# Performance work log

Hardware: AMD Instinct MI355X
Metric: run time of the kernel (lower is better)

Reference implementation:

```python
import jax, jax.numpy as jnp
from jax import lax
import numpy as np

DIM = 16
VOCAB = 18


def setup_inputs() -> dict:
    key = jax.random.key(0)
    ks = jax.random.split(key, 7)
    B, T = 4096, 2048
    x = jax.random.randint(ks[0], (B, T), 0, VOCAB, dtype=jnp.int64)
    emb = jax.random.normal(ks[1], (VOCAB, DIM), dtype=jnp.float32)
    W_w = jax.random.normal(ks[2], (DIM, DIM), dtype=jnp.float32) * (1.0 / np.sqrt(DIM))
    W_b = jax.random.normal(ks[3], (DIM,), dtype=jnp.float32) * 0.01
    U_w = jax.random.normal(ks[4], (DIM, DIM), dtype=jnp.float32) * (1.0 / np.sqrt(DIM))
    head_w = jax.random.normal(ks[5], (VOCAB, DIM), dtype=jnp.float32) * (1.0 / np.sqrt(DIM))
    head_b = jax.random.normal(ks[6], (VOCAB,), dtype=jnp.float32) * 0.01
    return {"x": x, "emb": emb, "W_w": W_w, "W_b": W_b, "U_w": U_w,
            "head_w": head_w, "head_b": head_b}


def reference(x, emb, W_w, W_b, U_w, head_w, head_b):
    # x: [B, T] int tokens; emb: [V, D]; W_w/U_w: [D, D]; head_w: [V, D]
    B, T = x.shape
    D = emb.shape[1]
    # Input-dependent term W(emb(x_t)) + b has no recurrence: precompute for all t.
    e = emb[x]                                   # [B, T, D] gather
    we = jnp.einsum('btd,kd->btk', e, W_w) + W_b  # [B, T, D]

    def step(h, we_t):
        # h_{t} = tanh(W emb(x_t) + b + U h_{t-1})
        h_new = jnp.tanh(we_t + h @ U_w.T)       # [B, D]
        return h_new, None

    h0 = jnp.zeros((B, D), dtype=emb.dtype)
    h_final, _ = lax.scan(step, h0, jnp.swapaxes(we, 0, 1))  # scan over T
    # head(h_final): [B, V]  (gates tensor in the original is all-ones and unused)
    return h_final @ head_w.T + head_b
```

## Files before the change

kernel.cpp:

```cpp
#include <hip/hip_runtime.h>
#include <cmath>

#define DIM 16
#define VOCAB 18
#define TLEN 2048
#define NBLK (TLEN / 64)
#define TWO_LOG2E 2.8853900817779268f

__device__ __forceinline__ float ldf(const void* p, int idx, int isbf) {
    if (isbf) {
        unsigned int w = ((const unsigned short*)p)[idx];
        return __uint_as_float(w << 16);
    }
    return ((const float*)p)[idx];
}

__global__ void detect_tok(const int* __restrict__ x32, int* __restrict__ flag) {
    int v = 0;
    for (int j = threadIdx.x; j < 4096; j += 64) v |= x32[2 * j + 1];
    unsigned long long any = __ballot(v != 0);
    if (threadIdx.x == 0) flag[0] = (any == 0ULL) ? 1 : 0;
}

__global__ void detect_f(const unsigned short* __restrict__ emb16,
                         int* __restrict__ flag) {
    int bad = 0;
    for (int j = threadIdx.x; j < VOCAB * DIM; j += 64) {
        unsigned short w = emb16[j];
        int e = (w >> 7) & 0xFF;
        if (!((e >= 90 && e <= 140) || (w & 0x7FFF) == 0)) bad = 1;
    }
    unsigned long long anybad = __ballot(bad);
    if (threadIdx.x == 0) flag[1] = (anybad == 0ULL) ? 1 : 0;
}

__global__ void wtab_kernel(const void* __restrict__ emb,
                            const void* __restrict__ W_w,
                            const void* __restrict__ W_b,
                            const int* __restrict__ flag,
                            float* __restrict__ wtab) {
    int tid = threadIdx.x;
    int isbf = flag[1];
    if (tid < VOCAB * DIM) {
        int v = tid >> 4, kk = tid & 15;
        float s = ldf(W_b, kk, isbf);
#pragma unroll
        for (int d = 0; d < DIM; ++d)
            s = fmaf(ldf(emb, v * DIM + d, isbf), ldf(W_w, kk * DIM + d, isbf), s);
        wtab[tid] = s;
    }
}

#define WSTR 19
#define SSTR 68

__global__ __launch_bounds__(256) void rnn_kernel(const int* __restrict__ x32,
                                                  const int* __restrict__ flag,
                                                  const float* __restrict__ wtab_g,
                                                  const void* __restrict__ U_w,
                                                  const void* __restrict__ head_w,
                                                  const void* __restrict__ head_b,
                                                  float* __restrict__ out) {
    __shared__ float wtabT[16 * WSTR];
    __shared__ float sU[DIM * DIM];
    __shared__ float lds_h[16][DIM];
    __shared__ int slab[2][16 * SSTR];

    const int tid = threadIdx.x;
    const int is64 = __builtin_amdgcn_readfirstlane(flag[0]);
    const int isbf = __builtin_amdgcn_readfirstlane(flag[1]);

    for (int i = tid; i < 16 * WSTR; i += 256) {
        int r = i / WSTR, v = i - r * WSTR;
        float val = 0.0f;
        if (v < VOCAB) {
            float rs = 0.0f;
#pragma unroll
            for (int d = 0; d < DIM; ++d) rs += ldf(U_w, r * DIM + d, isbf);
            val = (wtab_g[v * DIM + r] + rs) * TWO_LOG2E;
        }
        wtabT[i] = val;
    }
    for (int i = tid; i < DIM * DIM; i += 256) sU[i] = ldf(U_w, i, isbf);
    __syncthreads();

    const int lane = tid & 63;
    const int wave = tid >> 6;
    const int g16 = lane >> 4;
    const int k = lane & 15;
    const int e = (wave << 2) | g16;
    const int gelem = (blockIdx.x << 4) | e;

    int p = __builtin_amdgcn_mov_dpp(k, 0x121, 0xF, 0xF, true);
    int c = (p - k) & 15;

    float ur2[16];
#pragma unroll
    for (int j = 0; j < 16; ++j)
        ur2[j] = sU[(k << 4) | ((k + j * c) & 15)] * (-2.0f * TWO_LOG2E);

    const int wb = k * WSTR;

    const size_t tokbase = (size_t)gelem * TLEN + (k << 2);

    int* cur = &slab[0][e * SSTR];
    int* nxt = &slab[1][e * SSTR];

    int4 g0;
#define LOADG(G, B)                                                           \
    {                                                                         \
        if (is64) {                                                           \
            const int* pp = x32 + ((tokbase + ((size_t)(B) << 6)) << 1);      \
            int4 a = *(const int4*)pp;                                        \
            int4 bq = *(const int4*)(pp + 4);                                 \
            G = make_int4(a.x, a.z, bq.x, bq.z);                              \
        } else {                                                              \
            G = *(const int4*)(x32 + tokbase + ((size_t)(B) << 6));           \
        }                                                                     \
    }

    LOADG(g0, 0)
    *(int4*)(cur + (k << 2)) = g0;
    int4 gcur;
    LOADG(gcur, 1)

    int4 tA = *(const int4*)(cur + 0);
    int4 tB = *(const int4*)(cur + 4);
    float wq0 = wtabT[wb + tA.x];
    float wq1 = wtabT[wb + tA.y];
    float wq2 = wtabT[wb + tA.z];
    float wq3 = wtabT[wb + tA.w];

    float rst = 0.5f;

#define STEP(W, TN, WN)                                                        \
    {                                                                          \
        WN = wtabT[wb + (TN)];                                                 \
        float a0 = fmaf(ur2[0], rst, W);                                       \
        float a1, a2, a3;                                                      \
        asm("s_nop 1\n\t"                                                      \
            "v_mul_f32_dpp %[a1], %[r], %[u1] row_ror:1 row_mask:0xf bank_mask:0xf\n\t"  \
            "v_mul_f32_dpp %[a2], %[r], %[u2] row_ror:2 row_mask:0xf bank_mask:0xf\n\t"  \
            "v_mul_f32_dpp %[a3], %[r], %[u3] row_ror:3 row_mask:0xf bank_mask:0xf\n\t"  \
            "v_fmac_f32_dpp %[a0], %[r], %[u4] row_ror:4 row_mask:0xf bank_mask:0xf\n\t" \
            "v_fmac_f32_dpp %[a1], %[r], %[u5] row_ror:5 row_mask:0xf bank_mask:0xf\n\t" \
            "v_fmac_f32_dpp %[a2], %[r], %[u6] row_ror:6 row_mask:0xf bank_mask:0xf\n\t" \
            "v_fmac_f32_dpp %[a3], %[r], %[u7] row_ror:7 row_mask:0xf bank_mask:0xf\n\t" \
            "v_fmac_f32_dpp %[a0], %[r], %[u8] row_ror:8 row_mask:0xf bank_mask:0xf\n\t" \
            "v_fmac_f32_dpp %[a1], %[r], %[u9] row_ror:9 row_mask:0xf bank_mask:0xf\n\t" \
            "v_fmac_f32_dpp %[a2], %[r], %[u10] row_ror:10 row_mask:0xf bank_mask:0xf\n\t" \
            "v_fmac_f32_dpp %[a3], %[r], %[u11] row_ror:11 row_mask:0xf bank_mask:0xf\n\t" \
            "v_fmac_f32_dpp %[a0], %[r], %[u12] row_ror:12 row_mask:0xf bank_mask:0xf\n\t" \
            "v_fmac_f32_dpp %[a1], %[r], %[u13] row_ror:13 row_mask:0xf bank_mask:0xf\n\t" \
            "v_fmac_f32_dpp %[a2], %[r], %[u14] row_ror:14 row_mask:0xf bank_mask:0xf\n\t" \
            "v_fmac_f32_dpp %[a3], %[r], %[u15] row_ror:15 row_mask:0xf bank_mask:0xf"     \
            : [a0] "+v"(a0), [a1] "=&v"(a1), [a2] "=&v"(a2), [a3] "=&v"(a3)    \
            : [r] "v"(rst), [u1] "v"(ur2[1]), [u2] "v"(ur2[2]),                \
              [u3] "v"(ur2[3]), [u4] "v"(ur2[4]), [u5] "v"(ur2[5]),            \
              [u6] "v"(ur2[6]), [u7] "v"(ur2[7]), [u8] "v"(ur2[8]),            \
              [u9] "v"(ur2[9]), [u10] "v"(ur2[10]), [u11] "v"(ur2[11]),        \
              [u12] "v"(ur2[12]), [u13] "v"(ur2[13]), [u14] "v"(ur2[14]),      \
              [u15] "v"(ur2[15]));                                             \
        float S = (a0 + a1) + (a2 + a3);                                       \
        rst = __builtin_amdgcn_rcpf(__builtin_amdgcn_exp2f(S) + 1.0f);         \
    }

    for (int b = 0; b < NBLK; ++b) {
        *(int4*)(nxt + (k << 2)) = gcur;
        const int nb2 = (b + 2 < NBLK) ? b + 2 : NBLK - 1;
        LOADG(gcur, nb2)

#pragma unroll
        for (int gi = 0; gi < 16; ++gi) {
            int4 tC = (gi < 14) ? *(const int4*)(cur + ((gi + 2) << 2))
                                : *(const int4*)(nxt + ((gi - 14) << 2));

            float wn0, wn1, wn2, wn3;
            STEP(wq0, tB.x, wn0)
            STEP(wq1, tB.y, wn1)
            STEP(wq2, tB.z, wn2)
            STEP(wq3, tB.w, wn3)

            wq0 = wn0;
            wq1 = wn1;
            wq2 = wn2;
            wq3 = wn3;
            tB = tC;
        }
        int* tmp = cur;
        cur = nxt;
        nxt = tmp;
    }

    lds_h[e][k] = fmaf(-2.0f, rst, 1.0f);
    __syncthreads();

    for (int i = tid; i < 16 * VOCAB; i += 256) {
        int ee = i / VOCAB;
        int v = i - ee * VOCAB;
        float s = ldf(head_b, v, isbf);
#pragma unroll
        for (int d = 0; d < DIM; ++d)
            s = fmaf(lds_h[ee][d], ldf(head_w, (v << 4) + d, isbf), s);
        out[(size_t)((blockIdx.x << 4) | ee) * VOCAB + v] = s;
    }
}

extern "C" void kernel_launch(void* const* d_in, const int* in_sizes, int n_in,
                              void* d_out, int out_size, void* d_ws, size_t ws_size,
                              hipStream_t stream) {
    const int* x = (const int*)d_in[0];
    const void* emb = d_in[1];
    const void* W_w = d_in[2];
    const void* W_b = d_in[3];
    const void* U_w = d_in[4];
    const void* head_w = d_in[5];
    const void* head_b = d_in[6];

    float* wtab = (float*)d_ws;
    int* flag = (int*)((char*)d_ws + 4096);

    detect_tok<<<1, 64, 0, stream>>>(x, flag);
    detect_f<<<1, 64, 0, stream>>>((const unsigned short*)emb, flag);
    wtab_kernel<<<1, 320, 0, stream>>>(emb, W_w, W_b, flag, wtab);
    rnn_kernel<<<256, 256, 0, stream>>>(x, flag, wtab, U_w, head_w, head_b,
                                        (float*)d_out);
}
```

Before: 149.1 us.

## Interleave two independent recurrences per 16-lane group to hide latency

Each 16-lane group now carries two batch elements, A and B, and alternates their recurrence steps, so each wave runs two independent dependency chains. Blocks drop to 128 threads (2 waves) while still covering 16 elements per block. The goal is to hide the DPP/exp/rcp latency of the serial chain through instruction-level parallelism, since the grid of 256 blocks leaves the GPU underoccupied. The cost is half as many waves in flight and more registers per thread.

```diff
diff --git a/kernel.cpp b/kernel.cpp
--- a/kernel.cpp
+++ b/kernel.cpp
@@ -54,7 +54,7 @@
 #define WSTR 19
 #define SSTR 68
 
-__global__ __launch_bounds__(256) void rnn_kernel(const int* __restrict__ x32,
+__global__ __launch_bounds__(128) void rnn_kernel(const int* __restrict__ x32,
                                                   const int* __restrict__ flag,
                                                   const float* __restrict__ wtab_g,
                                                   const void* __restrict__ U_w,
@@ -70,7 +70,7 @@
     const int is64 = __builtin_amdgcn_readfirstlane(flag[0]);
     const int isbf = __builtin_amdgcn_readfirstlane(flag[1]);
 
-    for (int i = tid; i < 16 * WSTR; i += 256) {
+    for (int i = tid; i < 16 * WSTR; i += 128) {
         int r = i / WSTR, v = i - r * WSTR;
         float val = 0.0f;
         if (v < VOCAB) {
@@ -81,15 +81,17 @@
         }
         wtabT[i] = val;
     }
-    for (int i = tid; i < DIM * DIM; i += 256) sU[i] = ldf(U_w, i, isbf);
+    for (int i = tid; i < DIM * DIM; i += 128) sU[i] = ldf(U_w, i, isbf);
     __syncthreads();
 
     const int lane = tid & 63;
     const int wave = tid >> 6;
     const int g16 = lane >> 4;
     const int k = lane & 15;
-    const int e = (wave << 2) | g16;
-    const int gelem = (blockIdx.x << 4) | e;
+    const int eA = (wave << 3) | g16;
+    const int eB = eA + 4;
+    const int gelemA = (blockIdx.x << 4) | eA;
+    const int gelemB = (blockIdx.x << 4) | eB;
 
     int p = __builtin_amdgcn_mov_dpp(k, 0x121, 0xF, 0xF, true);
     int c = (p - k) & 15;
@@ -101,42 +103,50 @@
 
     const int wb = k * WSTR;
 
-    const size_t tokbase = (size_t)gelem * TLEN + (k << 2);
-
-    int* cur = &slab[0][e * SSTR];
-    int* nxt = &slab[1][e * SSTR];
-
-    int4 g0;
-#define LOADG(G, B)                                                           \
+    const size_t tokbaseA = (size_t)gelemA * TLEN + (k << 2);
+    const size_t tokbaseB = (size_t)gelemB * TLEN + (k << 2);
+
+    int* curA = &slab[0][eA * SSTR];
+    int* nxtA = &slab[1][eA * SSTR];
+    int* curB = &slab[0][eB * SSTR];
+    int* nxtB = &slab[1][eB * SSTR];
+
+#define LOADG(G, B, TOKBASE)                                                  \
     {                                                                         \
         if (is64) {                                                           \
-            const int* pp = x32 + ((tokbase + ((size_t)(B) << 6)) << 1);      \
+            const int* pp = x32 + (((TOKBASE) + ((size_t)(B) << 6)) << 1);    \
             int4 a = *(const int4*)pp;                                        \
             int4 bq = *(const int4*)(pp + 4);                                 \
             G = make_int4(a.x, a.z, bq.x, bq.z);                              \
         } else {                                                              \
-            G = *(const int4*)(x32 + tokbase + ((size_t)(B) << 6));           \
+            G = *(const int4*)(x32 + (TOKBASE) + ((size_t)(B) << 6));         \
         }                                                                     \
     }
 
-    LOADG(g0, 0)
-    *(int4*)(cur + (k << 2)) = g0;
-    int4 gcur;
-    LOADG(gcur, 1)
-
-    int4 tA = *(const int4*)(cur + 0);
-    int4 tB = *(const int4*)(cur + 4);
-    float wq0 = wtabT[wb + tA.x];
-    float wq1 = wtabT[wb + tA.y];
-    float wq2 = wtabT[wb + tA.z];
-    float wq3 = wtabT[wb + tA.w];
-
-    float rst = 0.5f;
-
-#define STEP(W, TN, WN)                                                        \
+    int4 g0;
+    LOADG(g0, 0, tokbaseA)
+    *(int4*)(curA + (k << 2)) = g0;
+    LOADG(g0, 0, tokbaseB)
+    *(int4*)(curB + (k << 2)) = g0;
+    int4 gcurA, gcurB;
+    LOADG(gcurA, 1, tokbaseA)
+    LOADG(gcurB, 1, tokbaseB)
+
+    int4 tA0 = *(const int4*)(curA + 0);
+    int4 tnA = *(const int4*)(curA + 4);
+    float wqA0 = wtabT[wb + tA0.x], wqA1 = wtabT[wb + tA0.y];
+    float wqA2 = wtabT[wb + tA0.z], wqA3 = wtabT[wb + tA0.w];
+    int4 tB0 = *(const int4*)(curB + 0);
+    int4 tnB = *(const int4*)(curB + 4);
+    float wqB0 = wtabT[wb + tB0.x], wqB1 = wtabT[wb + tB0.y];
+    float wqB2 = wtabT[wb + tB0.z], wqB3 = wtabT[wb + tB0.w];
+
+    float rstA = 0.5f, rstB = 0.5f;
+
+#define STEP(RST, W, TN, WN)                                                   \
     {                                                                          \
         WN = wtabT[wb + (TN)];                                                 \
-        float a0 = fmaf(ur2[0], rst, W);                                       \
+        float a0 = fmaf(ur2[0], RST, W);                                       \
         float a1, a2, a3;                                                      \
         asm("s_nop 1\n\t"                                                      \
             "v_mul_f32_dpp %[a1], %[r], %[u1] row_ror:1 row_mask:0xf bank_mask:0xf\n\t"  \
@@ -155,47 +165,54 @@
             "v_fmac_f32_dpp %[a2], %[r], %[u14] row_ror:14 row_mask:0xf bank_mask:0xf\n\t" \
             "v_fmac_f32_dpp %[a3], %[r], %[u15] row_ror:15 row_mask:0xf bank_mask:0xf"     \
             : [a0] "+v"(a0), [a1] "=&v"(a1), [a2] "=&v"(a2), [a3] "=&v"(a3)    \
-            : [r] "v"(rst), [u1] "v"(ur2[1]), [u2] "v"(ur2[2]),                \
+            : [r] "v"(RST), [u1] "v"(ur2[1]), [u2] "v"(ur2[2]),                \
               [u3] "v"(ur2[3]), [u4] "v"(ur2[4]), [u5] "v"(ur2[5]),            \
               [u6] "v"(ur2[6]), [u7] "v"(ur2[7]), [u8] "v"(ur2[8]),            \
               [u9] "v"(ur2[9]), [u10] "v"(ur2[10]), [u11] "v"(ur2[11]),        \
               [u12] "v"(ur2[12]), [u13] "v"(ur2[13]), [u14] "v"(ur2[14]),      \
               [u15] "v"(ur2[15]));                                             \
         float S = (a0 + a1) + (a2 + a3);                                       \
-        rst = __builtin_amdgcn_rcpf(__builtin_amdgcn_exp2f(S) + 1.0f);         \
+        RST = __builtin_amdgcn_rcpf(__builtin_amdgcn_exp2f(S) + 1.0f);         \
     }
 
     for (int b = 0; b < NBLK; ++b) {
-        *(int4*)(nxt + (k << 2)) = gcur;
+        *(int4*)(nxtA + (k << 2)) = gcurA;
+        *(int4*)(nxtB + (k << 2)) = gcurB;
         const int nb2 = (b + 2 < NBLK) ? b + 2 : NBLK - 1;
-        LOADG(gcur, nb2)
+        LOADG(gcurA, nb2, tokbaseA)
+        LOADG(gcurB, nb2, tokbaseB)
 
 #pragma unroll
         for (int gi = 0; gi < 16; ++gi) {
-            int4 tC = (gi < 14) ? *(const int4*)(cur + ((gi + 2) << 2))
-                                : *(const int4*)(nxt + ((gi - 14) << 2));
-
-            float wn0, wn1, wn2, wn3;
-            STEP(wq0, tB.x, wn0)
-            STEP(wq1, tB.y, wn1)
-            STEP(wq2, tB.z, wn2)
-            STEP(wq3, tB.w, wn3)
-
-            wq0 = wn0;
-            wq1 = wn1;
-            wq2 = wn2;
-            wq3 = wn3;
-            tB = tC;
+            int4 tCA = (gi < 14) ? *(const int4*)(curA + ((gi + 2) << 2))
+                                 : *(const int4*)(nxtA + ((gi - 14) << 2));
+            int4 tCB = (gi < 14) ? *(const int4*)(curB + ((gi + 2) << 2))
+                                 : *(const int4*)(nxtB + ((gi - 14) << 2));
+
+            float wnA0, wnA1, wnA2, wnA3, wnB0, wnB1, wnB2, wnB3;
+            STEP(rstA, wqA0, tnA.x, wnA0)
+            STEP(rstB, wqB0, tnB.x, wnB0)
+            STEP(rstA, wqA1, tnA.y, wnA1)
+            STEP(rstB, wqB1, tnB.y, wnB1)
+            STEP(rstA, wqA2, tnA.z, wnA2)
+            STEP(rstB, wqB2, tnB.z, wnB2)
+            STEP(rstA, wqA3, tnA.w, wnA3)
+            STEP(rstB, wqB3, tnB.w, wnB3)
+
+            wqA0 = wnA0; wqA1 = wnA1; wqA2 = wnA2; wqA3 = wnA3;
+            wqB0 = wnB0; wqB1 = wnB1; wqB2 = wnB2; wqB3 = wnB3;
+            tnA = tCA;
+            tnB = tCB;
         }
-        int* tmp = cur;
-        cur = nxt;
-        nxt = tmp;
-    }
-
-    lds_h[e][k] = fmaf(-2.0f, rst, 1.0f);
+        int* tmp = curA; curA = nxtA; nxtA = tmp;
+        tmp = curB; curB = nxtB; nxtB = tmp;
+    }
+
+    lds_h[eA][k] = fmaf(-2.0f, rstA, 1.0f);
+    lds_h[eB][k] = fmaf(-2.0f, rstB, 1.0f);
     __syncthreads();
 
-    for (int i = tid; i < 16 * VOCAB; i += 256) {
+    for (int i = tid; i < 16 * VOCAB; i += 128) {
         int ee = i / VOCAB;
         int v = i - ee * VOCAB;
         float s = ldf(head_b, v, isbf);
@@ -223,6 +240,6 @@
     detect_tok<<<1, 64, 0, stream>>>(x, flag);
     detect_f<<<1, 64, 0, stream>>>((const unsigned short*)emb, flag);
     wtab_kernel<<<1, 320, 0, stream>>>(emb, W_w, W_b, flag, wtab);
-    rnn_kernel<<<256, 256, 0, stream>>>(x, flag, wtab, U_w, head_w, head_b,
+    rnn_kernel<<<256, 128, 0, stream>>>(x, flag, wtab, U_w, head_w, head_b,
                                         (float*)d_out);
 }
```

After: 249.6 us. 67.4% more time.
